# Optimization experiments

Measured on AMD Instinct MI355X. Metric: run time of the kernel, lower is better.

Reference implementation:

```python
import jax, jax.numpy as jnp
import numpy as np

NL, D, H, DH, DFF, DIN, MAXLEN = 3, 128, 4, 32, 512, 64, 4096
B, L = 2, 2048


def setup_inputs() -> dict:
    key = jax.random.key(0)
    ks = jax.random.split(key, 10)
    def n(k, shape, s=0.02):
        return jax.random.normal(k, shape, jnp.float32) * s
    return dict(
        x=jax.random.normal(ks[0], (B, L, DIN), jnp.float32),
        embed_w=n(ks[1], (D, DIN)), embed_b=jnp.zeros((D,), jnp.float32),
        pos_emb=n(ks[2], (MAXLEN + 1, D)),
        cls=n(ks[3], (1, 1, D)),
        in_proj_w=n(ks[4], (NL, 3 * D, D)), in_proj_b=jnp.zeros((NL, 3 * D), jnp.float32),
        out_w=n(ks[5], (NL, D, D)), out_b=jnp.zeros((NL, D), jnp.float32),
        ln1_s=jnp.ones((NL, D), jnp.float32), ln1_b=jnp.zeros((NL, D), jnp.float32),
        ln2_s=jnp.ones((NL, D), jnp.float32), ln2_b=jnp.zeros((NL, D), jnp.float32),
        ff1_w=n(ks[6], (NL, DFF, D)), ff1_b=jnp.zeros((NL, DFF), jnp.float32),
        ff2_w=n(ks[7], (NL, D, DFF)), ff2_b=jnp.zeros((NL, D), jnp.float32),
        head_ln_s=jnp.ones((D,), jnp.float32), head_ln_b=jnp.zeros((D,), jnp.float32),
        head_w=n(ks[8], (1, D)), head_b=jnp.zeros((1,), jnp.float32),
    )


def _ln(x, s, b, eps=1e-5):
    m = x.mean(-1, keepdims=True)
    v = ((x - m) ** 2).mean(-1, keepdims=True)
    return (x - m) * jax.lax.rsqrt(v + eps) * s + b


def reference(x, embed_w, embed_b, pos_emb, cls, in_proj_w, in_proj_b, out_w, out_b,
              ln1_s, ln1_b, ln2_s, ln2_b, ff1_w, ff1_b, ff2_w, ff2_b,
              head_ln_s, head_ln_b, head_w, head_b):
    b, l, _ = x.shape
    # token embedding + positional embeddings at indices 1..L (0 reserved for CLS)
    h = x @ embed_w.T + embed_b + pos_emb[1:l + 1]            # [B,L,D]
    cls_tok = jnp.broadcast_to(cls + pos_emb[0], (b, 1, D))   # CLS gets pos_emb[0]
    h = jnp.concatenate([cls_tok, h], axis=1)                 # [B,S,D], S=L+1
    s = l + 1
    scale = 1.0 / np.sqrt(DH).astype(np.float32)
    for i in range(NL):  # norm_first encoder layers, eager MHA (dropout=0 / eval)
        hn = _ln(h, ln1_s[i], ln1_b[i])
        qkv = hn @ in_proj_w[i].T + in_proj_b[i]
        q, k, v = jnp.split(qkv, 3, axis=-1)
        q = q.reshape(b, s, H, DH)
        k = k.reshape(b, s, H, DH)
        v = v.reshape(b, s, H, DH)
        attn = jax.nn.softmax(jnp.einsum('bqhd,bkhd->bhqk', q, k) * scale, axis=-1)
        o = jnp.einsum('bhqk,bkhd->bqhd', attn, v).reshape(b, s, D)
        h = h + o @ out_w[i].T + out_b[i]
        hn = _ln(h, ln2_s[i], ln2_b[i])
        h = h + jax.nn.relu(hn @ ff1_w[i].T + ff1_b[i]) @ ff2_w[i].T + ff2_b[i]
    pooled = _ln(h[:, 0], head_ln_s, head_ln_b)               # CLS pooling
    return (pooled @ head_w.T + head_b)[:, 0]                 # [B]
```

## Files before the change

### kernel.cpp

```cpp
#include <hip/hip_runtime.h>

typedef unsigned short u16;
typedef float f32x4 __attribute__((ext_vector_type(4)));
typedef short short8 __attribute__((ext_vector_type(8)));

#define S_LEN 2049
#define SP    2112
#define BS    4098
#define MROWS 4112
#define KSPLIT 8

__device__ __forceinline__ float b2f(u16 u){
  unsigned int i = ((unsigned int)u) << 16; float f; __builtin_memcpy(&f, &i, 4); return f;
}
__device__ __forceinline__ u16 f2b(float f){
  unsigned int i; __builtin_memcpy(&i, &f, 4);
  unsigned int r = i + 0x7FFFu + ((i >> 16) & 1u);
  return (u16)(r >> 16);
}

enum {
  OFF_X = 0,            OFF_EW = 262144,  OFF_EB = 270336,  OFF_POS = 270464,
  OFF_CLS = 794880,     OFF_IPW = 795008, OFF_IPB = 942464, OFF_OW = 943616,
  OFF_OB = 992768,      OFF_L1S = 993152, OFF_L1B = 993536, OFF_L2S = 993920,
  OFF_L2B = 994304,     OFF_F1W = 994688, OFF_F1B = 1191296, OFF_F2W = 1192832,
  OFF_F2B = 1389440,    OFF_HLS = 1389824, OFF_HLB = 1389952, OFF_HW = 1390080,
  OFF_HB = 1390208,     OFF_END = 1390209, CANON_PAD = 1390216
};

struct CArgs { const void* s[21]; };

__global__ __launch_bounds__(256) void init_kernel(
    CArgs a, u16* __restrict__ dst, u16* __restrict__ qkv, float* __restrict__ h)
{
  const int offs[22] = {OFF_X,OFF_EW,OFF_EB,OFF_POS,OFF_CLS,OFF_IPW,OFF_IPB,OFF_OW,OFF_OB,
    OFF_L1S,OFF_L1B,OFF_L2S,OFF_L2B,OFF_F1W,OFF_F1B,OFF_F2W,OFF_F2B,OFF_HLS,OFF_HLB,
    OFF_HW,OFF_HB,OFF_END};
  int tid = blockIdx.x * 256 + threadIdx.x;
  if (tid < 24 * 63 * 32){
    int wb = tid / 2016;
    int r  = tid - wb * 2016;
    qkv[((size_t)wb * SP + S_LEN + r / 32) * 32 + (r & 31)] = 0;
  }
  if (tid < 256){
    int d = tid & 127, b = tid >> 7;
    h[(size_t)b * S_LEN * 128 + d] =
        ((const float*)a.s[4])[d] + ((const float*)a.s[3])[d];
  }
  if (tid >= OFF_END) return;
  int lo = 0, hi = 21;
  while (hi - lo > 1){ int mid = (lo + hi) >> 1; if (tid >= offs[mid]) lo = mid; else hi = mid; }
  dst[tid] = f2b(((const float*)a.s[lo])[tid - offs[lo]]);
}

__global__ __launch_bounds__(256) void embed_kernel(const u16* __restrict__ cw, float* __restrict__ h)
{
  int lane = threadIdx.x & 63;
  int wave = blockIdx.x * 4 + (threadIdx.x >> 6);
  int mt = wave >> 3, nt = wave & 7;
  int mi = lane & 15, quad = lane >> 4;
  const u16* Ap = cw + OFF_X + (size_t)(mt * 16 + mi) * 64 + quad * 8;
  const u16* Wp = cw + OFF_EW + (size_t)(nt * 16 + mi) * 64 + quad * 8;
  f32x4 acc = {0.f, 0.f, 0.f, 0.f};
#pragma unroll
  for (int kc = 0; kc < 2; kc++){
    short8 av = *(const short8*)(Ap + kc * 32);
    short8 wv = *(const short8*)(Wp + kc * 32);
    acc = __builtin_amdgcn_mfma_f32_16x16x32_bf16(av, wv, acc, 0, 0, 0);
  }
  int n = nt * 16 + mi;
  float ebv = b2f(cw[OFF_EB + n]);
#pragma unroll
  for (int r = 0; r < 4; r++){
    int m = mt * 16 + quad * 4 + r;
    int b = m >> 11, s = (m & 2047) + 1;
    h[((size_t)b * S_LEN + s) * 128 + n] =
        acc[r] + ebv + b2f(cw[OFF_POS + (size_t)s * 128 + n]);
  }
}

template<int N, int MODE>
__global__ __launch_bounds__(256, 4) void lngemm_kernel(
    const u16* __restrict__ cw, const float* __restrict__ h,
    const u16* __restrict__ g, const u16* __restrict__ be,
    const u16* __restrict__ W, const u16* __restrict__ bias, u16* __restrict__ out)
{
  constexpr int NT  = N / 16;
  constexpr int TOT = 257 * NT;
  int lane = threadIdx.x & 63;
  int wave = blockIdx.x * 4 + (threadIdx.x >> 6);
  if (wave >= TOT) return;
  int mt = wave / NT, nt = wave - mt * NT;
  int mi = lane & 15, quad = lane >> 4;
  const float* hrow = h + (size_t)(mt * 16 + mi) * 128 + quad * 8;
  float v[32];
  float sm = 0.f;
#pragma unroll
  for (int kc = 0; kc < 4; kc++){
    f32x4 x0 = *(const f32x4*)(hrow + kc * 32);
    f32x4 x1 = *(const f32x4*)(hrow + kc * 32 + 4);
#pragma unroll
    for (int j = 0; j < 4; j++){ v[kc*8+j] = x0[j]; v[kc*8+4+j] = x1[j]; }
    sm += x0[0]+x0[1]+x0[2]+x0[3]+x1[0]+x1[1]+x1[2]+x1[3];
  }
  sm += __shfl_xor(sm, 16, 64); sm += __shfl_xor(sm, 32, 64);
  float mean = sm * (1.f/128.f);
  float vv = 0.f;
#pragma unroll
  for (int j = 0; j < 32; j++){ float d = v[j] - mean; vv += d * d; }
  vv += __shfl_xor(vv, 16, 64); vv += __shfl_xor(vv, 32, 64);
  float rstd = rsqrtf(vv * (1.f/128.f) + 1e-5f);
  short8 af[4];
#pragma unroll
  for (int kc = 0; kc < 4; kc++){
    short8 gs = *(const short8*)(g  + kc * 32 + quad * 8);
    short8 bs = *(const short8*)(be + kc * 32 + quad * 8);
#pragma unroll
    for (int j = 0; j < 8; j++)
      af[kc][j] = (short)f2b((v[kc*8+j] - mean) * rstd * b2f((u16)gs[j]) + b2f((u16)bs[j]));
  }
  const u16* Wp = W + (size_t)(nt * 16 + mi) * 128 + quad * 8;
  f32x4 acc = {0.f, 0.f, 0.f, 0.f};
#pragma unroll
  for (int kc = 0; kc < 4; kc++){
    short8 wv = *(const short8*)(Wp + kc * 32);
    acc = __builtin_amdgcn_mfma_f32_16x16x32_bf16(af[kc], wv, acc, 0, 0, 0);
  }
  int n = nt * 16 + mi;
  float bv = b2f(bias[n]);
#pragma unroll
  for (int r = 0; r < 4; r++){
    int m = mt * 16 + quad * 4 + r;
    if (m >= BS) continue;
    float val = acc[r] + bv;
    if (MODE == 0){
      int which = n >> 7, d = n & 127, hd = d >> 5, dh = d & 31;
      int b_ = (m >= S_LEN) ? 1 : 0;
      int s  = m - b_ * S_LEN;
      out[(size_t)(((which * 2 + b_) * 4 + hd) * SP + s) * 32 + dh] = f2b(val);
    } else {
      out[(size_t)m * N + n] = f2b(val > 0.f ? val : 0.f);
    }
  }
}

template<int K>
__global__ __launch_bounds__(256) void gemm_res_kernel(
    const u16* __restrict__ A, const u16* __restrict__ W, const u16* __restrict__ bias,
    float* __restrict__ hres)
{
  constexpr int TOT = 257 * 8;
  int lane = threadIdx.x & 63;
  int wave = blockIdx.x * 4 + (threadIdx.x >> 6);
  if (wave >= TOT) return;
  int mt = wave >> 3, nt = wave & 7;
  int mi = lane & 15, quad = lane >> 4;
  const u16* Ap = A + (size_t)(mt * 16 + mi) * K + quad * 8;
  const u16* Wp = W + (size_t)(nt * 16 + mi) * K + quad * 8;
  f32x4 acc = {0.f, 0.f, 0.f, 0.f};
#pragma unroll
  for (int kc = 0; kc < K / 32; kc++){
    short8 a = *(const short8*)(Ap + kc * 32);
    short8 b = *(const short8*)(Wp + kc * 32);
    acc = __builtin_amdgcn_mfma_f32_16x16x32_bf16(a, b, acc, 0, 0, 0);
  }
  int n = nt * 16 + mi;
  float bv = b2f(bias[n]);
#pragma unroll
  for (int r = 0; r < 4; r++){
    int m = mt * 16 + quad * 4 + r;
    if (m >= BS) continue;
    hres[(size_t)m * 128 + n] += acc[r] + bv;
  }
}

__global__ __launch_bounds__(256, 4) void attn_kernel(
    const u16* __restrict__ qkv, float* __restrict__ Opart, float* __restrict__ Lpart)
{
  __shared__ u16 Kl[64 * 40];
  __shared__ u16 Vt[32 * 72];
  __shared__ u16 Pl[4][16 * 72];
  int tid = threadIdx.x;
  int lane = tid & 63, w = tid >> 6;
  int qt = blockIdx.x, bh = blockIdx.y, split = blockIdx.z;
  const u16* Qb = qkv + (size_t)bh * SP * 32;
  const u16* Kb = qkv + (size_t)(8 + bh) * SP * 32;
  const u16* Vb = qkv + (size_t)(16 + bh) * SP * 32;
  int mi = lane & 15, quad = lane >> 4;
  int q0 = qt * 64 + w * 16;
  short8 qf = *(const short8*)(Qb + (size_t)(q0 + mi) * 32 + quad * 8);
  f32x4 o0 = {0,0,0,0}, o1 = {0,0,0,0};
  float lp[4] = {0.f, 0.f, 0.f, 0.f};
  int c0 = (split * 33) >> 3, c1 = ((split + 1) * 33) >> 3;
  int kkey = tid >> 2, kdh = (tid & 3) * 8;
  int vdh = tid & 31, vgrp = tid >> 5;
  u16* Pw = Pl[w];
  for (int c = c0; c < c1; c++){
    int kb = c * 64;
    __syncthreads();
    *(short8*)&Kl[kkey * 40 + kdh] = *(const short8*)(Kb + (size_t)(kb + kkey) * 32 + kdh);
    {
      const u16* vb = Vb + (size_t)(kb + vgrp * 4) * 32 + vdh;
      ushort4 a, b;
      a.x = vb[0];    a.y = vb[32];   a.z = vb[64];   a.w = vb[96];
      b.x = vb[1024]; b.y = vb[1056]; b.z = vb[1088]; b.w = vb[1120];
      *(ushort4*)&Vt[vdh * 72 + vgrp * 4] = a;
      *(ushort4*)&Vt[vdh * 72 + (vgrp + 8) * 4] = b;
    }
    __syncthreads();
#pragma unroll
    for (int kt = 0; kt < 4; kt++){
      short8 kf = *(const short8*)&Kl[(kt * 16 + mi) * 40 + quad * 8];
      f32x4 z = {0,0,0,0};
      f32x4 s = __builtin_amdgcn_mfma_f32_16x16x32_bf16(qf, kf, z, 0, 0, 0);
      bool val = (kb + kt * 16 + mi) < S_LEN;
#pragma unroll
      for (int r = 0; r < 4; r++){
        float p = val ? exp2f(s[r] * 0.25503486f) : 0.f;
        lp[r] += p;
        Pw[(quad * 4 + r) * 72 + kt * 16 + mi] = f2b(p);
      }
    }
    short8 pf0 = *(const short8*)&Pw[mi * 72 + quad * 8];
    short8 pf1 = *(const short8*)&Pw[mi * 72 + 32 + quad * 8];
    short8 va0 = *(const short8*)&Vt[mi * 72 + quad * 8];
    short8 va1 = *(const short8*)&Vt[mi * 72 + 32 + quad * 8];
    short8 vb0 = *(const short8*)&Vt[(16 + mi) * 72 + quad * 8];
    short8 vb1 = *(const short8*)&Vt[(16 + mi) * 72 + 32 + quad * 8];
    o0 = __builtin_amdgcn_mfma_f32_16x16x32_bf16(pf0, va0, o0, 0, 0, 0);
    o0 = __builtin_amdgcn_mfma_f32_16x16x32_bf16(pf1, va1, o0, 0, 0, 0);
    o1 = __builtin_amdgcn_mfma_f32_16x16x32_bf16(pf0, vb0, o1, 0, 0, 0);
    o1 = __builtin_amdgcn_mfma_f32_16x16x32_bf16(pf1, vb1, o1, 0, 0, 0);
  }
#pragma unroll
  for (int r = 0; r < 4; r++){
    lp[r] += __shfl_xor(lp[r], 1, 64); lp[r] += __shfl_xor(lp[r], 2, 64);
    lp[r] += __shfl_xor(lp[r], 4, 64); lp[r] += __shfl_xor(lp[r], 8, 64);
  }
  size_t pb = ((size_t)qt * 8 + bh) * KSPLIT + split;
  float* Ob = Opart + pb * 2048 + (size_t)w * 16 * 32;
#pragma unroll
  for (int r = 0; r < 4; r++){
    Ob[(quad * 4 + r) * 32 + mi]      = o0[r];
    Ob[(quad * 4 + r) * 32 + 16 + mi] = o1[r];
  }
  if (mi == 0){
#pragma unroll
    for (int r = 0; r < 4; r++)
      Lpart[pb * 64 + w * 16 + quad * 4 + r] = lp[r];
  }
}

__global__ __launch_bounds__(256) void attn_reduce_kernel(
    const float* __restrict__ Opart, const float* __restrict__ Lpart, u16* __restrict__ aout)
{
  __shared__ float linv[64];
  int qt = blockIdx.x, bh = blockIdx.y;
  int tid = threadIdx.x;
  size_t pb0 = ((size_t)qt * 8 + bh) * KSPLIT;
  if (tid < 64){
    float ls = 0.f;
#pragma unroll
    for (int s = 0; s < KSPLIT; s++) ls += Lpart[(pb0 + s) * 64 + tid];
    linv[tid] = 1.f / fmaxf(ls, 1e-30f);
  }
  __syncthreads();
  int e = tid * 8;
  f32x4 s0 = {0,0,0,0}, s1 = {0,0,0,0};
#pragma unroll
  for (int s = 0; s < KSPLIT; s++){
    const float* base = Opart + (pb0 + s) * 2048 + e;
    s0 += *(const f32x4*)base;
    s1 += *(const f32x4*)(base + 4);
  }
  int q = e >> 5;
  int tok = qt * 64 + q;
  if (tok < S_LEN){
    int bq = bh >> 2, hh = bh & 3;
    float inv = linv[q];
    ushort4 w0, w1;
    w0.x = f2b(s0[0]*inv); w0.y = f2b(s0[1]*inv); w0.z = f2b(s0[2]*inv); w0.w = f2b(s0[3]*inv);
    w1.x = f2b(s1[0]*inv); w1.y = f2b(s1[1]*inv); w1.z = f2b(s1[2]*inv); w1.w = f2b(s1[3]*inv);
    u16* dst = aout + ((size_t)bq * S_LEN + tok) * 128 + hh * 32 + (e & 31);
    *(ushort4*)dst = w0;
    *(ushort4*)(dst + 4) = w1;
  }
}

__global__ __launch_bounds__(128) void head_kernel(
    const float* __restrict__ h, const u16* __restrict__ cw, float* __restrict__ out)
{
  __shared__ float red[128];
  int tid = threadIdx.x;
  for (int b = 0; b < 2; b++){
    float e = h[(size_t)b * S_LEN * 128 + tid];
    red[tid] = e; __syncthreads();
    for (int st = 64; st > 0; st >>= 1){ if (tid < st) red[tid] += red[tid + st]; __syncthreads(); }
    float mean = red[0] * (1.f/128.f); __syncthreads();
    float d = e - mean; red[tid] = d * d; __syncthreads();
    for (int st = 64; st > 0; st >>= 1){ if (tid < st) red[tid] += red[tid + st]; __syncthreads(); }
    float rstd = rsqrtf(red[0] * (1.f/128.f) + 1e-5f); __syncthreads();
    float val = d * rstd * b2f(cw[OFF_HLS + tid]) + b2f(cw[OFF_HLB + tid]);
    red[tid] = val * b2f(cw[OFF_HW + tid]); __syncthreads();
    for (int st = 64; st > 0; st >>= 1){ if (tid < st) red[tid] += red[tid + st]; __syncthreads(); }
    if (tid == 0) out[b] = red[0] + b2f(cw[OFF_HB]);
    __syncthreads();
  }
}

extern "C" void kernel_launch(void* const* d_in, const int* in_sizes, int n_in,
                              void* d_out, int out_size, void* d_ws, size_t ws_size,
                              hipStream_t stream)
{
  char* ws = (char*)d_ws;
  u16* cw     = (u16*)ws;    ws += (size_t)CANON_PAD * 2;
  float* h    = (float*)ws;  ws += (size_t)MROWS * 128 * 4;
  u16* qkv    = (u16*)ws;    ws += (size_t)24 * SP * 32 * 2;
  u16* aout   = (u16*)ws;    ws += (size_t)MROWS * 128 * 2;
  u16* f1     = (u16*)ws;    ws += (size_t)MROWS * 512 * 2;
  float* Opart= (float*)ws;  ws += (size_t)33 * 8 * KSPLIT * 2048 * 4;
  float* Lpart= (float*)ws;  ws += (size_t)33 * 8 * KSPLIT * 64 * 4;

  CArgs ca;
  for (int i = 0; i < 21; i++) ca.s[i] = d_in[i];

  init_kernel<<<dim3((OFF_END + 255) / 256), dim3(256), 0, stream>>>(ca, cw, qkv, h);
  embed_kernel<<<dim3(512), dim3(256), 0, stream>>>(cw, h);
  for (int l = 0; l < 3; l++){
    lngemm_kernel<384, 0><<<dim3(1542), dim3(256), 0, stream>>>(
        cw, h, cw + OFF_L1S + l * 128, cw + OFF_L1B + l * 128,
        cw + OFF_IPW + (size_t)l * 384 * 128, cw + OFF_IPB + l * 384, qkv);
    attn_kernel<<<dim3(33, 8, KSPLIT), dim3(256), 0, stream>>>(qkv, Opart, Lpart);
    attn_reduce_kernel<<<dim3(33, 8), dim3(256), 0, stream>>>(Opart, Lpart, aout);
    gemm_res_kernel<128><<<dim3(514), dim3(256), 0, stream>>>(
        aout, cw + OFF_OW + (size_t)l * 128 * 128, cw + OFF_OB + l * 128, h);
    lngemm_kernel<512, 2><<<dim3(2056), dim3(256), 0, stream>>>(
        cw, h, cw + OFF_L2S + l * 128, cw + OFF_L2B + l * 128,
        cw + OFF_F1W + (size_t)l * 512 * 128, cw + OFF_F1B + l * 512, f1);
    gemm_res_kernel<512><<<dim3(514), dim3(256), 0, stream>>>(
        f1, cw + OFF_F2W + (size_t)l * 128 * 512, cw + OFF_F2B + l * 128, h);
  }
  head_kernel<<<dim3(1), dim3(128), 0, stream>>>(h, cw, (float*)d_out);
}
```

Measured before the change: 335.2 us.

## Fuse attention split reduction with output projection and pad residual layout per batch

The activation buffer is re-laid out with each batch padded to 2112 rows, so the padding rows are zero-initialized and every GEMM can drop its bounds checks. The separate attention-reduce kernel and the out-projection GEMM are merged into one kernel, which rebuilds a 16-row tile in LDS and multiplies it directly, removing the aout round trip and one launch. The attention loop now register-prefetches the next K/V chunk while the current one is computed, and uses a hardware exp2 intrinsic with cheaper bf16 rounding. In exchange, the padded rows add extra compute, and the approximate rounding slightly changes numerics.

```diff
diff --git a/kernel.cpp b/kernel.cpp
--- a/kernel.cpp
+++ b/kernel.cpp
@@ -5,9 +5,9 @@
 typedef short short8 __attribute__((ext_vector_type(8)));
 
 #define S_LEN 2049
-#define SP    2112
-#define BS    4098
-#define MROWS 4112
+#define SPAD  2112
+#define MP    4224
+#define MT    264
 #define KSPLIT 8
 
 __device__ __forceinline__ float b2f(u16 u){
@@ -18,6 +18,15 @@
   unsigned int r = i + 0x7FFFu + ((i >> 16) & 1u);
   return (u16)(r >> 16);
 }
+__device__ __forceinline__ u16 f2b_fast(float f){
+  unsigned int i; __builtin_memcpy(&i, &f, 4);
+  return (u16)((i + 0x8000u) >> 16);
+}
+#if __has_builtin(__builtin_amdgcn_exp2f)
+#define EXP2F(x) __builtin_amdgcn_exp2f(x)
+#else
+#define EXP2F(x) exp2f(x)
+#endif
 
 enum {
   OFF_X = 0,            OFF_EW = 262144,  OFF_EB = 270336,  OFF_POS = 270464,
@@ -31,21 +40,20 @@
 struct CArgs { const void* s[21]; };
 
 __global__ __launch_bounds__(256) void init_kernel(
-    CArgs a, u16* __restrict__ dst, u16* __restrict__ qkv, float* __restrict__ h)
+    CArgs a, u16* __restrict__ dst, float* __restrict__ h)
 {
   const int offs[22] = {OFF_X,OFF_EW,OFF_EB,OFF_POS,OFF_CLS,OFF_IPW,OFF_IPB,OFF_OW,OFF_OB,
     OFF_L1S,OFF_L1B,OFF_L2S,OFF_L2B,OFF_F1W,OFF_F1B,OFF_F2W,OFF_F2B,OFF_HLS,OFF_HLB,
     OFF_HW,OFF_HB,OFF_END};
   int tid = blockIdx.x * 256 + threadIdx.x;
-  if (tid < 24 * 63 * 32){
-    int wb = tid / 2016;
-    int r  = tid - wb * 2016;
-    qkv[((size_t)wb * SP + S_LEN + r / 32) * 32 + (r & 31)] = 0;
-  }
   if (tid < 256){
     int d = tid & 127, b = tid >> 7;
-    h[(size_t)b * S_LEN * 128 + d] =
+    h[(size_t)b * SPAD * 128 + d] =
         ((const float*)a.s[4])[d] + ((const float*)a.s[3])[d];
+  }
+  if (tid < 2 * 63 * 128){
+    int b = tid / 8064, r = (tid % 8064) / 128, d = tid & 127;
+    h[((size_t)b * SPAD + S_LEN + r) * 128 + d] = 0.f;
   }
   if (tid >= OFF_END) return;
   int lo = 0, hi = 21;
@@ -74,22 +82,20 @@
   for (int r = 0; r < 4; r++){
     int m = mt * 16 + quad * 4 + r;
     int b = m >> 11, s = (m & 2047) + 1;
-    h[((size_t)b * S_LEN + s) * 128 + n] =
+    h[((size_t)b * SPAD + s) * 128 + n] =
         acc[r] + ebv + b2f(cw[OFF_POS + (size_t)s * 128 + n]);
   }
 }
 
 template<int N, int MODE>
 __global__ __launch_bounds__(256, 4) void lngemm_kernel(
-    const u16* __restrict__ cw, const float* __restrict__ h,
+    const float* __restrict__ h,
     const u16* __restrict__ g, const u16* __restrict__ be,
     const u16* __restrict__ W, const u16* __restrict__ bias, u16* __restrict__ out)
 {
-  constexpr int NT  = N / 16;
-  constexpr int TOT = 257 * NT;
+  constexpr int NT = N / 16;
   int lane = threadIdx.x & 63;
   int wave = blockIdx.x * 4 + (threadIdx.x >> 6);
-  if (wave >= TOT) return;
   int mt = wave / NT, nt = wave - mt * NT;
   int mi = lane & 15, quad = lane >> 4;
   const float* hrow = h + (size_t)(mt * 16 + mi) * 128 + quad * 8;
@@ -131,13 +137,12 @@
 #pragma unroll
   for (int r = 0; r < 4; r++){
     int m = mt * 16 + quad * 4 + r;
-    if (m >= BS) continue;
     float val = acc[r] + bv;
     if (MODE == 0){
       int which = n >> 7, d = n & 127, hd = d >> 5, dh = d & 31;
-      int b_ = (m >= S_LEN) ? 1 : 0;
-      int s  = m - b_ * S_LEN;
-      out[(size_t)(((which * 2 + b_) * 4 + hd) * SP + s) * 32 + dh] = f2b(val);
+      int b_ = (m >= SPAD) ? 1 : 0;
+      int s  = m - b_ * SPAD;
+      out[(size_t)(((which * 2 + b_) * 4 + hd) * SPAD + s) * 32 + dh] = f2b(val);
     } else {
       out[(size_t)m * N + n] = f2b(val > 0.f ? val : 0.f);
     }
@@ -149,10 +154,8 @@
     const u16* __restrict__ A, const u16* __restrict__ W, const u16* __restrict__ bias,
     float* __restrict__ hres)
 {
-  constexpr int TOT = 257 * 8;
   int lane = threadIdx.x & 63;
   int wave = blockIdx.x * 4 + (threadIdx.x >> 6);
-  if (wave >= TOT) return;
   int mt = wave >> 3, nt = wave & 7;
   int mi = lane & 15, quad = lane >> 4;
   const u16* Ap = A + (size_t)(mt * 16 + mi) * K + quad * 8;
@@ -169,7 +172,6 @@
 #pragma unroll
   for (int r = 0; r < 4; r++){
     int m = mt * 16 + quad * 4 + r;
-    if (m >= BS) continue;
     hres[(size_t)m * 128 + n] += acc[r] + bv;
   }
 }
@@ -183,9 +185,9 @@
   int tid = threadIdx.x;
   int lane = tid & 63, w = tid >> 6;
   int qt = blockIdx.x, bh = blockIdx.y, split = blockIdx.z;
-  const u16* Qb = qkv + (size_t)bh * SP * 32;
-  const u16* Kb = qkv + (size_t)(8 + bh) * SP * 32;
-  const u16* Vb = qkv + (size_t)(16 + bh) * SP * 32;
+  const u16* Qb = qkv + (size_t)bh * SPAD * 32;
+  const u16* Kb = qkv + (size_t)(8 + bh) * SPAD * 32;
+  const u16* Vb = qkv + (size_t)(16 + bh) * SPAD * 32;
   int mi = lane & 15, quad = lane >> 4;
   int q0 = qt * 64 + w * 16;
   short8 qf = *(const short8*)(Qb + (size_t)(q0 + mi) * 32 + quad * 8);
@@ -195,19 +197,27 @@
   int kkey = tid >> 2, kdh = (tid & 3) * 8;
   int vdh = tid & 31, vgrp = tid >> 5;
   u16* Pw = Pl[w];
+  short8 kreg = *(const short8*)(Kb + (size_t)(c0 * 64 + kkey) * 32 + kdh);
+  ushort4 va, vb;
+  {
+    const u16* vp = Vb + (size_t)(c0 * 64 + vgrp * 4) * 32 + vdh;
+    va.x = vp[0];    va.y = vp[32];   va.z = vp[64];   va.w = vp[96];
+    vb.x = vp[1024]; vb.y = vp[1056]; vb.z = vp[1088]; vb.w = vp[1120];
+  }
   for (int c = c0; c < c1; c++){
-    int kb = c * 64;
     __syncthreads();
-    *(short8*)&Kl[kkey * 40 + kdh] = *(const short8*)(Kb + (size_t)(kb + kkey) * 32 + kdh);
+    *(short8*)&Kl[kkey * 40 + kdh] = kreg;
+    *(ushort4*)&Vt[vdh * 72 + vgrp * 4] = va;
+    *(ushort4*)&Vt[vdh * 72 + (vgrp + 8) * 4] = vb;
     {
-      const u16* vb = Vb + (size_t)(kb + vgrp * 4) * 32 + vdh;
-      ushort4 a, b;
-      a.x = vb[0];    a.y = vb[32];   a.z = vb[64];   a.w = vb[96];
-      b.x = vb[1024]; b.y = vb[1056]; b.z = vb[1088]; b.w = vb[1120];
-      *(ushort4*)&Vt[vdh * 72 + vgrp * 4] = a;
-      *(ushort4*)&Vt[vdh * 72 + (vgrp + 8) * 4] = b;
+      int cn = (c + 1 < c1) ? c + 1 : c;
+      kreg = *(const short8*)(Kb + (size_t)(cn * 64 + kkey) * 32 + kdh);
+      const u16* vp = Vb + (size_t)(cn * 64 + vgrp * 4) * 32 + vdh;
+      va.x = vp[0];    va.y = vp[32];   va.z = vp[64];   va.w = vp[96];
+      vb.x = vp[1024]; vb.y = vp[1056]; vb.z = vp[1088]; vb.w = vp[1120];
     }
     __syncthreads();
+    int kb = c * 64;
 #pragma unroll
     for (int kt = 0; kt < 4; kt++){
       short8 kf = *(const short8*)&Kl[(kt * 16 + mi) * 40 + quad * 8];
@@ -216,21 +226,21 @@
       bool val = (kb + kt * 16 + mi) < S_LEN;
 #pragma unroll
       for (int r = 0; r < 4; r++){
-        float p = val ? exp2f(s[r] * 0.25503486f) : 0.f;
+        float p = val ? EXP2F(s[r] * 0.25503486f) : 0.f;
         lp[r] += p;
-        Pw[(quad * 4 + r) * 72 + kt * 16 + mi] = f2b(p);
+        Pw[(quad * 4 + r) * 72 + kt * 16 + mi] = f2b_fast(p);
       }
     }
     short8 pf0 = *(const short8*)&Pw[mi * 72 + quad * 8];
     short8 pf1 = *(const short8*)&Pw[mi * 72 + 32 + quad * 8];
-    short8 va0 = *(const short8*)&Vt[mi * 72 + quad * 8];
-    short8 va1 = *(const short8*)&Vt[mi * 72 + 32 + quad * 8];
-    short8 vb0 = *(const short8*)&Vt[(16 + mi) * 72 + quad * 8];
-    short8 vb1 = *(const short8*)&Vt[(16 + mi) * 72 + 32 + quad * 8];
-    o0 = __builtin_amdgcn_mfma_f32_16x16x32_bf16(pf0, va0, o0, 0, 0, 0);
-    o0 = __builtin_amdgcn_mfma_f32_16x16x32_bf16(pf1, va1, o0, 0, 0, 0);
-    o1 = __builtin_amdgcn_mfma_f32_16x16x32_bf16(pf0, vb0, o1, 0, 0, 0);
-    o1 = __builtin_amdgcn_mfma_f32_16x16x32_bf16(pf1, vb1, o1, 0, 0, 0);
+    short8 wa0 = *(const short8*)&Vt[mi * 72 + quad * 8];
+    short8 wa1 = *(const short8*)&Vt[mi * 72 + 32 + quad * 8];
+    short8 wb0 = *(const short8*)&Vt[(16 + mi) * 72 + quad * 8];
+    short8 wb1 = *(const short8*)&Vt[(16 + mi) * 72 + 32 + quad * 8];
+    o0 = __builtin_amdgcn_mfma_f32_16x16x32_bf16(pf0, wa0, o0, 0, 0, 0);
+    o0 = __builtin_amdgcn_mfma_f32_16x16x32_bf16(pf1, wa1, o0, 0, 0, 0);
+    o1 = __builtin_amdgcn_mfma_f32_16x16x32_bf16(pf0, wb0, o1, 0, 0, 0);
+    o1 = __builtin_amdgcn_mfma_f32_16x16x32_bf16(pf1, wb1, o1, 0, 0, 0);
   }
 #pragma unroll
   for (int r = 0; r < 4; r++){
@@ -251,39 +261,50 @@
   }
 }
 
-__global__ __launch_bounds__(256) void attn_reduce_kernel(
-    const float* __restrict__ Opart, const float* __restrict__ Lpart, u16* __restrict__ aout)
-{
-  __shared__ float linv[64];
-  int qt = blockIdx.x, bh = blockIdx.y;
+__global__ __launch_bounds__(512, 2) void redout_kernel(
+    const float* __restrict__ Opart, const float* __restrict__ Lpart,
+    const u16* __restrict__ W, const u16* __restrict__ bias, float* __restrict__ hres)
+{
+  __shared__ u16 Al[16 * 136];
   int tid = threadIdx.x;
-  size_t pb0 = ((size_t)qt * 8 + bh) * KSPLIT;
-  if (tid < 64){
+  int mt = blockIdx.x;
+  int b = mt / 132, tle = mt % 132;
+  int qt = tle >> 2, w = tle & 3;
+  {
+    int hd = tid >> 7;
+    int e  = (tid * 4) & 511;
+    int r  = e >> 5, dh0 = e & 31;
+    size_t base = (((size_t)qt * 8 + (b * 4 + hd)) * KSPLIT) * 2048 + w * 512 + r * 32 + dh0;
+    f32x4 acc = {0,0,0,0};
     float ls = 0.f;
 #pragma unroll
-    for (int s = 0; s < KSPLIT; s++) ls += Lpart[(pb0 + s) * 64 + tid];
-    linv[tid] = 1.f / fmaxf(ls, 1e-30f);
+    for (int sp = 0; sp < KSPLIT; sp++){
+      acc += *(const f32x4*)(Opart + base + (size_t)sp * 2048);
+      ls  += Lpart[(((size_t)qt * 8 + (b * 4 + hd)) * KSPLIT + sp) * 64 + w * 16 + r];
+    }
+    float inv = 1.f / fmaxf(ls, 1e-30f);
+    ushort4 pk;
+    pk.x = f2b(acc[0] * inv); pk.y = f2b(acc[1] * inv);
+    pk.z = f2b(acc[2] * inv); pk.w = f2b(acc[3] * inv);
+    *(ushort4*)&Al[r * 136 + hd * 32 + dh0] = pk;
   }
   __syncthreads();
-  int e = tid * 8;
-  f32x4 s0 = {0,0,0,0}, s1 = {0,0,0,0};
-#pragma unroll
-  for (int s = 0; s < KSPLIT; s++){
-    const float* base = Opart + (pb0 + s) * 2048 + e;
-    s0 += *(const f32x4*)base;
-    s1 += *(const f32x4*)(base + 4);
-  }
-  int q = e >> 5;
-  int tok = qt * 64 + q;
-  if (tok < S_LEN){
-    int bq = bh >> 2, hh = bh & 3;
-    float inv = linv[q];
-    ushort4 w0, w1;
-    w0.x = f2b(s0[0]*inv); w0.y = f2b(s0[1]*inv); w0.z = f2b(s0[2]*inv); w0.w = f2b(s0[3]*inv);
-    w1.x = f2b(s1[0]*inv); w1.y = f2b(s1[1]*inv); w1.z = f2b(s1[2]*inv); w1.w = f2b(s1[3]*inv);
-    u16* dst = aout + ((size_t)bq * S_LEN + tok) * 128 + hh * 32 + (e & 31);
-    *(ushort4*)dst = w0;
-    *(ushort4*)(dst + 4) = w1;
+  int lane = tid & 63, nt = tid >> 6;
+  int mi = lane & 15, quad = lane >> 4;
+  const u16* Wp = W + (size_t)(nt * 16 + mi) * 128 + quad * 8;
+  f32x4 acc = {0.f, 0.f, 0.f, 0.f};
+#pragma unroll
+  for (int kc = 0; kc < 4; kc++){
+    short8 af = *(const short8*)&Al[mi * 136 + kc * 32 + quad * 8];
+    short8 wv = *(const short8*)(Wp + kc * 32);
+    acc = __builtin_amdgcn_mfma_f32_16x16x32_bf16(af, wv, acc, 0, 0, 0);
+  }
+  int n = nt * 16 + mi;
+  float bv = b2f(bias[n]);
+#pragma unroll
+  for (int r = 0; r < 4; r++){
+    int m = mt * 16 + quad * 4 + r;
+    hres[(size_t)m * 128 + n] += acc[r] + bv;
   }
 }
 
@@ -293,7 +314,7 @@
   __shared__ float red[128];
   int tid = threadIdx.x;
   for (int b = 0; b < 2; b++){
-    float e = h[(size_t)b * S_LEN * 128 + tid];
+    float e = h[(size_t)b * SPAD * 128 + tid];
     red[tid] = e; __syncthreads();
     for (int st = 64; st > 0; st >>= 1){ if (tid < st) red[tid] += red[tid + st]; __syncthreads(); }
     float mean = red[0] * (1.f/128.f); __syncthreads();
@@ -314,30 +335,28 @@
 {
   char* ws = (char*)d_ws;
   u16* cw     = (u16*)ws;    ws += (size_t)CANON_PAD * 2;
-  float* h    = (float*)ws;  ws += (size_t)MROWS * 128 * 4;
-  u16* qkv    = (u16*)ws;    ws += (size_t)24 * SP * 32 * 2;
-  u16* aout   = (u16*)ws;    ws += (size_t)MROWS * 128 * 2;
-  u16* f1     = (u16*)ws;    ws += (size_t)MROWS * 512 * 2;
+  float* h    = (float*)ws;  ws += (size_t)MP * 128 * 4;
+  u16* qkv    = (u16*)ws;    ws += (size_t)24 * SPAD * 32 * 2;
+  u16* f1     = (u16*)ws;    ws += (size_t)MP * 512 * 2;
   float* Opart= (float*)ws;  ws += (size_t)33 * 8 * KSPLIT * 2048 * 4;
   float* Lpart= (float*)ws;  ws += (size_t)33 * 8 * KSPLIT * 64 * 4;
 
   CArgs ca;
   for (int i = 0; i < 21; i++) ca.s[i] = d_in[i];
 
-  init_kernel<<<dim3((OFF_END + 255) / 256), dim3(256), 0, stream>>>(ca, cw, qkv, h);
+  init_kernel<<<dim3((OFF_END + 255) / 256), dim3(256), 0, stream>>>(ca, cw, h);
   embed_kernel<<<dim3(512), dim3(256), 0, stream>>>(cw, h);
   for (int l = 0; l < 3; l++){
-    lngemm_kernel<384, 0><<<dim3(1542), dim3(256), 0, stream>>>(
-        cw, h, cw + OFF_L1S + l * 128, cw + OFF_L1B + l * 128,
+    lngemm_kernel<384, 0><<<dim3(MT * 24 / 4), dim3(256), 0, stream>>>(
+        h, cw + OFF_L1S + l * 128, cw + OFF_L1B + l * 128,
         cw + OFF_IPW + (size_t)l * 384 * 128, cw + OFF_IPB + l * 384, qkv);
     attn_kernel<<<dim3(33, 8, KSPLIT), dim3(256), 0, stream>>>(qkv, Opart, Lpart);
-    attn_reduce_kernel<<<dim3(33, 8), dim3(256), 0, stream>>>(Opart, Lpart, aout);
-    gemm_res_kernel<128><<<dim3(514), dim3(256), 0, stream>>>(
-        aout, cw + OFF_OW + (size_t)l * 128 * 128, cw + OFF_OB + l * 128, h);
-    lngemm_kernel<512, 2><<<dim3(2056), dim3(256), 0, stream>>>(
-        cw, h, cw + OFF_L2S + l * 128, cw + OFF_L2B + l * 128,
+    redout_kernel<<<dim3(MT), dim3(512), 0, stream>>>(
+        Opart, Lpart, cw + OFF_OW + (size_t)l * 128 * 128, cw + OFF_OB + l * 128, h);
+    lngemm_kernel<512, 2><<<dim3(MT * 32 / 4), dim3(256), 0, stream>>>(
+        h, cw + OFF_L2S + l * 128, cw + OFF_L2B + l * 128,
         cw + OFF_F1W + (size_t)l * 512 * 128, cw + OFF_F1B + l * 512, f1);
-    gemm_res_kernel<512><<<dim3(514), dim3(256), 0, stream>>>(
+    gemm_res_kernel<512><<<dim3(MT * 8 / 4), dim3(256), 0, stream>>>(
         f1, cw + OFF_F2W + (size_t)l * 128 * 512, cw + OFF_F2B + l * 128, h);
   }
   head_kernel<<<dim3(1), dim3(128), 0, stream>>>(h, cw, (float*)d_out);
```

New measurement: 319.2 us. -4.8%, faster.
